# Optimization experiments

Measured on AMD Instinct MI355X. Metric: run time of the kernel, lower is better.

The kernel has to match this reference:

```python
import jax, jax.numpy as jnp
import numpy as np

N_RES, N_SSE, N_DOM = 20000, 2000, 40
E_RES, E_SSE, E_DOM = 300000, 8000, 160
F_IN, H, D, OUT = 1302, 4, 128, 256
SSE_IN = D + 3 + 1
NEG_SLOPE = 0.2   # PyG GATConv default negative_slope
BN_EPS = 1e-5


def setup_inputs() -> dict:
    key = jax.random.key(0)
    ks = jax.random.split(key, 20)
    p = lambda i, shape: jax.random.normal(ks[i], shape, dtype=jnp.float32) * 0.05
    return {
        'x_res': jax.random.normal(ks[0], (N_RES, F_IN), dtype=jnp.float32),
        'edge_index_res': jax.random.randint(ks[1], (2, E_RES), 0, N_RES),
        'edge_index_sse': jax.random.randint(ks[2], (2, E_SSE), 0, N_SSE),
        'edge_index_dom': jax.random.randint(ks[3], (2, E_DOM), 0, N_DOM),
        'res_sse_id': jnp.arange(N_RES) // (N_RES // N_SSE),  # contiguous SSE groups
        'sse_ss_type': jax.random.randint(ks[4], (N_SSE,), 0, 3),
        'n_dom': N_DOM,
        'W1': p(5, (F_IN, H * D)), 'a_src1': p(6, (H, D)), 'a_dst1': p(7, (H, D)), 'b1': jnp.zeros(H * D),
        'g1': jnp.ones(H * D), 'be1': jnp.zeros(H * D),
        'W2': p(8, (H * D, H * D)), 'a_src2': p(9, (H, D)), 'a_dst2': p(10, (H, D)), 'b2': jnp.zeros(D),
        'g2': jnp.ones(D), 'be2': jnp.zeros(D),
        'Ws': p(11, (SSE_IN, H * D)), 'a_srcs': p(12, (H, D)), 'a_dsts': p(13, (H, D)), 'bs': jnp.zeros(D),
        'gs': jnp.ones(D), 'bes': jnp.zeros(D),
        'Wd': p(14, (D, OUT)), 'bd': jnp.zeros(OUT), 'gd': jnp.ones(OUT), 'bed': jnp.zeros(OUT),
        'Wproj': p(15, (D, OUT)), 'bproj': jnp.zeros(OUT),
        'Wread': p(16, (2 * OUT, OUT)), 'bread': jnp.zeros(OUT),
    }


def _bn(x, g, b):
    # BatchNorm1d with batch statistics (training-mode math, dropout disabled)
    m = x.mean(0)
    v = ((x - m) ** 2).mean(0)
    return (x - m) * jax.lax.rsqrt(v + BN_EPS) * g + b


def _gat(x, src, dst, W, a_src, a_dst, bias, concat):
    # PyG GATConv: gather -> leaky_relu -> scatter-softmax over dst -> scatter-add
    N = x.shape[0]
    loops = jnp.arange(N)
    s = jnp.concatenate([src, loops])
    d = jnp.concatenate([dst, loops])
    h = (x @ W).reshape(N, H, D)               # [N,H,D]
    es = (h * a_src).sum(-1)                    # [N,H]
    ed = (h * a_dst).sum(-1)
    e = jax.nn.leaky_relu(es[s] + ed[d], NEG_SLOPE)          # [E+N,H]
    mx = jax.ops.segment_max(e, d, num_segments=N)
    ex = jnp.exp(e - mx[d])
    den = jax.ops.segment_sum(ex, d, num_segments=N)
    alpha = ex / (den[d] + 1e-16)
    out = jax.ops.segment_sum(alpha[:, :, None] * h[s], d, num_segments=N)  # [N,H,D]
    out = out.reshape(N, H * D) if concat else out.mean(1)
    return out + bias


def _gcn(x, src, dst, W, bias):
    # PyG GCNConv with symmetric normalization and self loops
    N = x.shape[0]
    loops = jnp.arange(N)
    s = jnp.concatenate([src, loops])
    d = jnp.concatenate([dst, loops])
    deg = jax.ops.segment_sum(jnp.ones(s.shape[0], x.dtype), d, num_segments=N)
    dis = jax.lax.rsqrt(jnp.maximum(deg, 1e-12))
    coef = dis[s] * dis[d]
    h = x @ W
    return jax.ops.segment_sum(coef[:, None] * h[s], d, num_segments=N) + bias


def reference(x_res, edge_index_res, res_sse_id, sse_ss_type, edge_index_sse,
              edge_index_dom, n_dom,
              W1, a_src1, a_dst1, b1, g1, be1,
              W2, a_src2, a_dst2, b2, g2, be2,
              Ws, a_srcs, a_dsts, bs, gs, bes,
              Wd, bd, gd, bed, Wproj, bproj, Wread, bread):
    n_res = x_res.shape[0]
    n_sse = sse_ss_type.shape[0]
    # --- Level 1: residue GATs ---
    x = _gat(x_res, edge_index_res[0], edge_index_res[1], W1, a_src1, a_dst1, b1, True)
    x = jax.nn.relu(_bn(x, g1, be1))
    x = _gat(x, edge_index_res[0], edge_index_res[1], W2, a_src2, a_dst2, b2, False)
    x = jax.nn.relu(_bn(x, g2, be2))
    # --- pool residues -> SSEs (segment mean + ss one-hot + relative length) ---
    cnt = jax.ops.segment_sum(jnp.ones(n_res, x.dtype), res_sse_id, num_segments=n_sse)
    pooled = jax.ops.segment_sum(x, res_sse_id, num_segments=n_sse) / jnp.maximum(cnt, 1.0)[:, None]
    onehot = jax.nn.one_hot(sse_ss_type, 3, dtype=x.dtype)
    length = (cnt / n_res)[:, None]
    x_sse = jnp.concatenate([pooled, onehot, length], axis=1)   # [N_sse, 132]
    # --- Level 2: SSE GAT (concat=False) ---
    x_sse = _gat(x_sse, edge_index_sse[0], edge_index_sse[1], Ws, a_srcs, a_dsts, bs, False)
    x_sse = jax.nn.relu(_bn(x_sse, gs, bes))
    # --- pool SSEs -> domains (equal contiguous partition, remainder to last) ---
    spd = n_sse // n_dom
    dom_id = jnp.minimum(jnp.arange(n_sse) // spd, n_dom - 1)
    dcnt = jax.ops.segment_sum(jnp.ones(n_sse, x_sse.dtype), dom_id, num_segments=n_dom)
    x_dom = jax.ops.segment_sum(x_sse, dom_id, num_segments=n_dom) / dcnt[:, None]
    # --- Level 3: domain GCN ---
    x_dom = _gcn(x_dom, edge_index_dom[0], edge_index_dom[1], Wd, bd)
    x_dom = jax.nn.relu(_bn(x_dom, gd, bed))
    # --- readout ---
    sse_global = x_sse.mean(0)                 # [128]
    sse_proj = sse_global @ Wproj + bproj      # [256]
    dom_mean = x_dom.mean(0)                   # [256]
    out = jnp.concatenate([sse_proj, dom_mean]) @ Wread + bread
    out = out / jnp.maximum(jnp.linalg.norm(out), 1e-12)
    return out
```

## Files before the change

### kernel.cpp

```cpp
#include <hip/hip_runtime.h>
#include <math.h>

#define NRES   20000
#define NSSE   2000
#define NDOM   40
#define FIN    1302
#define NHEAD  4
#define DDIM   128
#define HD     512
#define OUTD   256
#define SSEIN  132
#define BN_EPS 1e-5f
#define KP1    1312

typedef _Float16 f16;
typedef __attribute__((ext_vector_type(8))) _Float16 f16x8;
typedef __attribute__((ext_vector_type(4))) float f32x4;

__device__ __forceinline__ float leaky(float v) { return v > 0.f ? v : 0.2f * v; }

__global__ __launch_bounds__(256) void split_rows(const float* __restrict__ X,
                                                  f16* __restrict__ hi, f16* __restrict__ lo,
                                                  int M, int K, int Kpad) {
    long slots = (long)M * (Kpad >> 3);
    long stride = (long)gridDim.x * blockDim.x;
    for (long s = (long)blockIdx.x * blockDim.x + threadIdx.x; s < slots; s += stride) {
        int m = (int)(s / (Kpad >> 3));
        int kc = (int)(s % (Kpad >> 3)) << 3;
        f16x8 h, l;
#pragma unroll
        for (int j = 0; j < 8; ++j) {
            int k = kc + j;
            float v = (k < K) ? X[(long)m * K + k] : 0.f;
            f16 hh = (f16)v;
            h[j] = hh;
            l[j] = (f16)(v - (float)hh);
        }
        long o = ((long)m * Kpad + kc);
        *(f16x8*)&hi[o] = h;
        *(f16x8*)&lo[o] = l;
    }
}

__global__ __launch_bounds__(256) void split_w_t(const float* __restrict__ W,
                                                 f16* __restrict__ hi, f16* __restrict__ lo,
                                                 int K, int N, int Kpad) {
    long total = (long)N * Kpad;
    long stride = (long)gridDim.x * blockDim.x;
    for (long i = (long)blockIdx.x * blockDim.x + threadIdx.x; i < total; i += stride) {
        int n = (int)(i / Kpad), k = (int)(i % Kpad);
        float v = (k < K) ? W[(long)k * N + n] : 0.f;
        f16 h = (f16)v;
        hi[i] = h;
        lo[i] = (f16)(v - (float)h);
    }
}

__global__ __launch_bounds__(256) void bn_apply_split(const float* __restrict__ x,
                                                      const float* __restrict__ ab,
                                                      f16* __restrict__ hi, f16* __restrict__ lo,
                                                      long total, int C) {
    long stride = (long)gridDim.x * blockDim.x;
    for (long i = (long)blockIdx.x * blockDim.x + threadIdx.x; i < total; i += stride) {
        int c = (int)(i % C);
        float v = fmaxf(0.f, x[i] * ab[c] + ab[C + c]);
        f16 h = (f16)v;
        hi[i] = h;
        lo[i] = (f16)(v - (float)h);
    }
}

__global__ __launch_bounds__(256) void mfma_gemm(const f16* __restrict__ Ahi,
                                                 const f16* __restrict__ Alo,
                                                 const f16* __restrict__ Bthi,
                                                 const f16* __restrict__ Btlo,
                                                 float* __restrict__ C,
                                                 int M, int RB, int Kpad) {
    int bid = blockIdx.x;
    int xcd = bid & 7;
    int q = bid >> 3;
    int x = q & 3;
    int y = (q >> 2) * 8 + xcd;
    if (y >= RB) return;

    __shared__ f16 As[2][128][40];
    __shared__ f16 Bs[2][128][40];
    int t = threadIdx.x;
    int w = t >> 6, l = t & 63;
    int wr = w >> 1, wc = w & 1;
    int row0 = y * 128, col0 = x * 128;

    f32x4 acc[4][4] = {};

    for (int k0 = 0; k0 < Kpad; k0 += 32) {
#pragma unroll
        for (int r = 0; r < 2; ++r) {
            int s = t + (r << 8);
            int row = s >> 2, kc = (s & 3) << 3;
            int grow = row0 + row; if (grow >= M) grow = M - 1;
            long gia = (long)grow * Kpad + k0 + kc;
            *(f16x8*)&As[0][row][kc] = *(const f16x8*)&Ahi[gia];
            *(f16x8*)&As[1][row][kc] = *(const f16x8*)&Alo[gia];
            long gib = (long)(col0 + row) * Kpad + k0 + kc;
            *(f16x8*)&Bs[0][row][kc] = *(const f16x8*)&Bthi[gib];
            *(f16x8*)&Bs[1][row][kc] = *(const f16x8*)&Btlo[gib];
        }
        __syncthreads();

        int lr = l & 15, ks = (l >> 4) << 3;
        f16x8 ah[4], al[4], bh[4], bl[4];
#pragma unroll
        for (int fi = 0; fi < 4; ++fi) {
            int row = wr * 64 + fi * 16 + lr;
            ah[fi] = *(const f16x8*)&As[0][row][ks];
            al[fi] = *(const f16x8*)&As[1][row][ks];
        }
#pragma unroll
        for (int fj = 0; fj < 4; ++fj) {
            int col = wc * 64 + fj * 16 + lr;
            bh[fj] = *(const f16x8*)&Bs[0][col][ks];
            bl[fj] = *(const f16x8*)&Bs[1][col][ks];
        }
#pragma unroll
        for (int fi = 0; fi < 4; ++fi)
#pragma unroll
            for (int fj = 0; fj < 4; ++fj) {
                acc[fi][fj] = __builtin_amdgcn_mfma_f32_16x16x32_f16(ah[fi], bh[fj], acc[fi][fj], 0, 0, 0);
                acc[fi][fj] = __builtin_amdgcn_mfma_f32_16x16x32_f16(ah[fi], bl[fj], acc[fi][fj], 0, 0, 0);
                acc[fi][fj] = __builtin_amdgcn_mfma_f32_16x16x32_f16(al[fi], bh[fj], acc[fi][fj], 0, 0, 0);
            }
        __syncthreads();
    }
    int lr = l & 15, lq = l >> 4;
#pragma unroll
    for (int fi = 0; fi < 4; ++fi)
#pragma unroll
        for (int fj = 0; fj < 4; ++fj)
#pragma unroll
            for (int r = 0; r < 4; ++r) {
                int row = row0 + wr * 64 + fi * 16 + lq * 4 + r;
                int col = col0 + wc * 64 + fj * 16 + lr;
                if (row < M) C[(long)row * 512 + col] = acc[fi][fj][r];
            }
}

__global__ __launch_bounds__(256) void sgemm64(const float* __restrict__ A,
                                               const float* __restrict__ B,
                                               float* __restrict__ C,
                                               int M, int N, int K) {
    __shared__ float As[16][68];
    __shared__ float Bs[16][68];
    int t = threadIdx.x;
    int tx = t & 15, ty = t >> 4;
    int row0 = blockIdx.y * 64, col0 = blockIdx.x * 64;
    float acc[4][4] = {};
    for (int k0 = 0; k0 < K; k0 += 16) {
#pragma unroll
        for (int i = 0; i < 4; ++i) {
            int idx = t * 4 + i;
            int r = idx >> 4, kk = idx & 15;
            int gr = row0 + r, gk = k0 + kk;
            As[kk][r] = (gr < M && gk < K) ? A[(long)gr * K + gk] : 0.f;
        }
#pragma unroll
        for (int i = 0; i < 4; ++i) {
            int idx = t * 4 + i;
            int kk = idx >> 6, c = idx & 63;
            int gk = k0 + kk, gc = col0 + c;
            Bs[kk][c] = (gk < K && gc < N) ? B[(long)gk * N + gc] : 0.f;
        }
        __syncthreads();
#pragma unroll
        for (int kk = 0; kk < 16; ++kk) {
            float a[4], b[4];
#pragma unroll
            for (int i = 0; i < 4; ++i) a[i] = As[kk][ty * 4 + i];
#pragma unroll
            for (int j = 0; j < 4; ++j) b[j] = Bs[kk][tx * 4 + j];
#pragma unroll
            for (int i = 0; i < 4; ++i)
#pragma unroll
                for (int j = 0; j < 4; ++j) acc[i][j] += a[i] * b[j];
        }
        __syncthreads();
    }
#pragma unroll
    for (int i = 0; i < 4; ++i) {
        int r = row0 + ty * 4 + i;
        if (r >= M) continue;
#pragma unroll
        for (int j = 0; j < 4; ++j) {
            int c = col0 + tx * 4 + j;
            if (c < N) C[(long)r * N + c] = acc[i][j];
        }
    }
}

__global__ void count_deg(const int* __restrict__ dst, int E, int* __restrict__ deg) {
    int i = blockIdx.x * blockDim.x + threadIdx.x;
    if (i < E) atomicAdd(&deg[dst[i]], 1);
}

__global__ __launch_bounds__(256) void exclusive_scan(const int* __restrict__ deg,
                                                      int* __restrict__ row_ptr, int N) {
    __shared__ int part[256];
    __shared__ int base[257];
    int t = threadIdx.x;
    int chunk = (N + 255) / 256;
    int lo = t * chunk, hi = min(lo + chunk, N);
    if (lo > N) lo = N;
    if (hi > N) hi = N;
    int s = 0;
    for (int i = lo; i < hi; ++i) s += deg[i];
    part[t] = s;
    __syncthreads();
    if (t == 0) {
        int r = 0;
        for (int i = 0; i < 256; ++i) { base[i] = r; r += part[i]; }
        base[256] = r;
    }
    __syncthreads();
    int run = base[t];
    for (int i = lo; i < hi; ++i) { row_ptr[i] = run; run += deg[i]; }
    if (t == 0) row_ptr[N] = base[256];
}

__global__ void csr_fill(const int* __restrict__ src, const int* __restrict__ dst, int E,
                         const int* __restrict__ row_ptr, int* __restrict__ cursor,
                         int* __restrict__ col) {
    int i = blockIdx.x * blockDim.x + threadIdx.x;
    if (i < E) {
        int d = dst[i];
        int p = row_ptr[d] + atomicAdd(&cursor[d], 1);
        col[p] = src[i];
    }
}

__global__ __launch_bounds__(256) void att_scores(const float* __restrict__ h,
                                                  const float* __restrict__ asrc,
                                                  const float* __restrict__ adst,
                                                  float* __restrict__ es,
                                                  float* __restrict__ ed, int N) {
    int wid = threadIdx.x >> 6, lane = threadIdx.x & 63;
    int n = blockIdx.x * 4 + wid;
    if (n >= N) return;
    const float* hr = h + (long)n * HD;
    float ps[NHEAD], pd[NHEAD];
#pragma unroll
    for (int hh = 0; hh < NHEAD; ++hh) {
        float s = 0.f, d = 0.f;
#pragma unroll
        for (int j = 0; j < 2; ++j) {
            int c = hh * DDIM + lane + j * 64;
            float v = hr[c];
            s += v * asrc[c];
            d += v * adst[c];
        }
        ps[hh] = s; pd[hh] = d;
    }
#pragma unroll
    for (int off = 32; off > 0; off >>= 1) {
#pragma unroll
        for (int hh = 0; hh < NHEAD; ++hh) {
            ps[hh] += __shfl_xor(ps[hh], off);
            pd[hh] += __shfl_xor(pd[hh], off);
        }
    }
    if (lane == 0) {
#pragma unroll
        for (int hh = 0; hh < NHEAD; ++hh) {
            es[n * NHEAD + hh] = ps[hh];
            ed[n * NHEAD + hh] = pd[hh];
        }
    }
}

__global__ __launch_bounds__(256) void gat_aggregate(const float* __restrict__ h,
                                                     const float* __restrict__ es,
                                                     const float* __restrict__ ed,
                                                     const int* __restrict__ row_ptr,
                                                     const int* __restrict__ col,
                                                     const float* __restrict__ bias,
                                                     float* __restrict__ out,
                                                     int N, int concat) {
    int n = blockIdx.x;
    int t = threadIdx.x;
    int lane = t & 63, wid = t >> 6;
    int s0 = row_ptr[n], s1 = row_ptr[n + 1];

    float edv[NHEAD], vself[NHEAD];
#pragma unroll
    for (int hh = 0; hh < NHEAD; ++hh) {
        edv[hh] = ed[n * NHEAD + hh];
        vself[hh] = leaky(es[n * NHEAD + hh] + edv[hh]);
    }
    __shared__ float sred[4][NHEAD];
    __shared__ float m[NHEAD], den[NHEAD];

    float lm[NHEAD] = {-1e30f, -1e30f, -1e30f, -1e30f};
    for (int k = s0 + t; k < s1; k += 256) {
        int sn = col[k];
#pragma unroll
        for (int hh = 0; hh < NHEAD; ++hh)
            lm[hh] = fmaxf(lm[hh], leaky(es[sn * NHEAD + hh] + edv[hh]));
    }
#pragma unroll
    for (int off = 32; off > 0; off >>= 1)
#pragma unroll
        for (int hh = 0; hh < NHEAD; ++hh) lm[hh] = fmaxf(lm[hh], __shfl_xor(lm[hh], off));
    if (lane == 0)
#pragma unroll
        for (int hh = 0; hh < NHEAD; ++hh) sred[wid][hh] = lm[hh];
    __syncthreads();
    if (t < NHEAD) {
        float mm = vself[t];
#pragma unroll
        for (int w = 0; w < 4; ++w) mm = fmaxf(mm, sred[w][t]);
        m[t] = mm;
    }
    __syncthreads();
    float mh[NHEAD];
#pragma unroll
    for (int hh = 0; hh < NHEAD; ++hh) mh[hh] = m[hh];

    float ls[NHEAD] = {0.f, 0.f, 0.f, 0.f};
    for (int k = s0 + t; k < s1; k += 256) {
        int sn = col[k];
#pragma unroll
        for (int hh = 0; hh < NHEAD; ++hh)
            ls[hh] += expf(leaky(es[sn * NHEAD + hh] + edv[hh]) - mh[hh]);
    }
#pragma unroll
    for (int off = 32; off > 0; off >>= 1)
#pragma unroll
        for (int hh = 0; hh < NHEAD; ++hh) ls[hh] += __shfl_xor(ls[hh], off);
    if (lane == 0)
#pragma unroll
        for (int hh = 0; hh < NHEAD; ++hh) sred[wid][hh] = ls[hh];
    __syncthreads();
    if (t < NHEAD)
        den[t] = sred[0][t] + sred[1][t] + sred[2][t] + sred[3][t] + expf(vself[t] - m[t]);
    __syncthreads();
    float inv[NHEAD];
#pragma unroll
    for (int hh = 0; hh < NHEAD; ++hh) inv[hh] = 1.f / (den[hh] + 1e-16f);

    int d0 = t, d1 = t + 256;
    int h0 = t >> 7, h1 = h0 + 2;
    float acc0, acc1;
    {
        float a0 = expf(vself[h0] - mh[h0]) * inv[h0];
        float a1 = expf(vself[h1] - mh[h1]) * inv[h1];
        acc0 = a0 * h[(long)n * HD + d0];
        acc1 = a1 * h[(long)n * HD + d1];
    }
    __shared__ float alph[64 * NHEAD];
    for (int base = s0; base < s1; base += 64) {
        int cnt = min(64, s1 - base);
        if (t < cnt * NHEAD) {
            int e = t >> 2, hh = t & 3;
            int sn = col[base + e];
            float v = leaky(es[sn * NHEAD + hh] + edv[hh]);
            alph[(e << 2) | hh] = expf(v - mh[hh]) * inv[hh];
        }
        __syncthreads();
        for (int e = 0; e < cnt; ++e) {
            int sn = col[base + e];
            const float* hs = h + (long)sn * HD;
            acc0 += alph[(e << 2) | h0] * hs[d0];
            acc1 += alph[(e << 2) | h1] * hs[d1];
        }
        __syncthreads();
    }

    if (concat) {
        out[(long)n * HD + d0] = acc0 + bias[d0];
        out[(long)n * HD + d1] = acc1 + bias[d1];
    } else {
        __shared__ float accs[HD];
        accs[d0] = acc0;
        accs[d1] = acc1;
        __syncthreads();
        if (t < DDIM)
            out[(long)n * DDIM + t] =
                (accs[t] + accs[t + 128] + accs[t + 256] + accs[t + 384]) * 0.25f + bias[t];
    }
}

__global__ __launch_bounds__(256) void bn_stats(const float* __restrict__ x,
                                                float* __restrict__ sums, long total, int C) {
    long gid = (long)blockIdx.x * blockDim.x + threadIdx.x;
    long stride = (long)gridDim.x * blockDim.x;
    int c = (int)(gid % C);
    float s = 0.f, s2 = 0.f;
    for (long i = gid; i < total; i += stride) {
        float v = x[i];
        s += v; s2 += v * v;
    }
    atomicAdd(&sums[c], s);
    atomicAdd(&sums[C + c], s2);
}

__global__ void bn_finalize(const float* __restrict__ sums, const float* __restrict__ g,
                            const float* __restrict__ be, float* __restrict__ ab,
                            float invN, int C) {
    int c = blockIdx.x * blockDim.x + threadIdx.x;
    if (c < C) {
        float mean = sums[c] * invN;
        float var = sums[C + c] * invN - mean * mean;
        float sc = g[c] * rsqrtf(var + BN_EPS);
        ab[c] = sc;
        ab[C + c] = be[c] - mean * sc;
    }
}

__global__ __launch_bounds__(256) void bn_apply_relu(const float* __restrict__ x,
                                                     const float* __restrict__ ab,
                                                     float* __restrict__ y, long total, int C) {
    long gid = (long)blockIdx.x * blockDim.x + threadIdx.x;
    long stride = (long)gridDim.x * blockDim.x;
    for (long i = gid; i < total; i += stride) {
        int c = (int)(i % C);
        y[i] = fmaxf(0.f, x[i] * ab[c] + ab[C + c]);
    }
}

__global__ void count_res(const int* __restrict__ sid, float* __restrict__ cnt, int Nr) {
    int i = blockIdx.x * blockDim.x + threadIdx.x;
    if (i < Nr) atomicAdd(&cnt[sid[i]], 1.f);
}

__global__ __launch_bounds__(256) void pool_res(const float* __restrict__ x,
                                                const int* __restrict__ sid,
                                                float* __restrict__ pooled, int Nr) {
    long total = (long)Nr * DDIM;
    long stride = (long)gridDim.x * blockDim.x;
    for (long i = (long)blockIdx.x * blockDim.x + threadIdx.x; i < total; i += stride) {
        int n = (int)(i / DDIM), c = (int)(i % DDIM);
        atomicAdd(&pooled[(long)sid[n] * DDIM + c], x[i]);
    }
}

__global__ void build_xsse(const float* __restrict__ pooled, const float* __restrict__ cnt,
                           const int* __restrict__ sstype, float* __restrict__ xsse, int Ns) {
    int i = blockIdx.x * blockDim.x + threadIdx.x;
    if (i >= Ns * SSEIN) return;
    int s = i / SSEIN, j = i % SSEIN;
    float c = cnt[s];
    float v;
    if (j < DDIM) v = pooled[(long)s * DDIM + j] / fmaxf(c, 1.f);
    else if (j < DDIM + 3) v = (sstype[s] == (j - DDIM)) ? 1.f : 0.f;
    else v = c / (float)NRES;
    xsse[i] = v;
}

__global__ void pool_dom(const float* __restrict__ x, float* __restrict__ xdom) {
    int d = blockIdx.x, c = threadIdx.x;
    int spd = NSSE / NDOM;
    int r0 = d * spd;
    int r1 = (d == NDOM - 1) ? NSSE : r0 + spd;
    float acc = 0.f;
    for (int r = r0; r < r1; ++r) acc += x[(long)r * DDIM + c];
    xdom[d * DDIM + c] = acc / (float)(r1 - r0);
}

__global__ __launch_bounds__(256) void gcn_prep(const int* __restrict__ src,
                                                const int* __restrict__ dst, int E,
                                                float* __restrict__ dis) {
    __shared__ float degL[NDOM];
    int t = threadIdx.x;
    if (t < NDOM) degL[t] = 1.f;
    __syncthreads();
    for (int e = t; e < E; e += blockDim.x) atomicAdd(&degL[dst[e]], 1.f);
    __syncthreads();
    if (t < NDOM) dis[t] = rsqrtf(fmaxf(degL[t], 1e-12f));
}

__global__ void gcn_agg(const float* __restrict__ hdom, const int* __restrict__ src,
                        const int* __restrict__ dst, int E, const float* __restrict__ dis,
                        const float* __restrict__ bd, float* __restrict__ outd) {
    int n = blockIdx.x, c = threadIdx.x;
    float dn = dis[n];
    float acc = dn * dn * hdom[n * OUTD + c];
    for (int e = 0; e < E; ++e)
        if (dst[e] == n) acc += dis[src[e]] * dn * hdom[src[e] * OUTD + c];
    outd[n * OUTD + c] = acc + bd[c];
}

__global__ void bn_small_relu(const float* __restrict__ x, const float* __restrict__ g,
                              const float* __restrict__ be, float* __restrict__ y,
                              int N, int C) {
    int c = threadIdx.x;
    if (c >= C) return;
    float s = 0.f, s2 = 0.f;
#pragma unroll 8
    for (int r = 0; r < N; ++r) {
        float v = x[r * C + c];
        s += v; s2 += v * v;
    }
    float mean = s / N;
    float var = s2 / N - mean * mean;
    float sc = g[c] * rsqrtf(var + BN_EPS);
    float sh = be[c] - mean * sc;
#pragma unroll 8
    for (int r = 0; r < N; ++r) y[r * C + c] = fmaxf(0.f, x[r * C + c] * sc + sh);
}

__global__ __launch_bounds__(256) void col_sum_atomic(const float* __restrict__ x,
                                                      float* __restrict__ out,
                                                      long total, int C) {
    long gid = (long)blockIdx.x * blockDim.x + threadIdx.x;
    long stride = (long)gridDim.x * blockDim.x;
    int c = (int)(gid % C);
    float s = 0.f;
    for (long i = gid; i < total; i += stride) s += x[i];
    atomicAdd(&out[c], s);
}

__global__ __launch_bounds__(256) void readout(const float* __restrict__ sse_sum,
                                               float invNs,
                                               const float* __restrict__ xdom_bn,
                                               const float* __restrict__ Wproj,
                                               const float* __restrict__ bproj,
                                               const float* __restrict__ Wread,
                                               const float* __restrict__ bread,
                                               float* __restrict__ out) {
    int c = threadIdx.x;
    __shared__ float v[2 * OUTD];
    float s = 0.f;
#pragma unroll 8
    for (int k = 0; k < DDIM; ++k) s += sse_sum[k] * Wproj[k * OUTD + c];
    v[c] = s * invNs + bproj[c];
    float dm = 0.f;
#pragma unroll 8
    for (int r = 0; r < NDOM; ++r) dm += xdom_bn[r * OUTD + c];
    v[OUTD + c] = dm / (float)NDOM;
    __syncthreads();
    float o = bread[c];
#pragma unroll 8
    for (int k = 0; k < 2 * OUTD; ++k) o += v[k] * Wread[k * OUTD + c];
    __shared__ float sq[256];
    sq[c] = o * o;
    __syncthreads();
    for (int off = 128; off > 0; off >>= 1) {
        if (c < off) sq[c] += sq[c + off];
        __syncthreads();
    }
    float scale = 1.f / fmaxf(sqrtf(sq[0]), 1e-12f);
    out[c] = o * scale;
}

extern "C" void kernel_launch(void* const* d_in, const int* in_sizes, int n_in,
                              void* d_out, int out_size, void* d_ws, size_t ws_size,
                              hipStream_t stream) {
    const float* x_res = (const float*)d_in[0];
    const int* ei_res = (const int*)d_in[1];
    const int* ei_sse = (const int*)d_in[2];
    const int* ei_dom = (const int*)d_in[3];
    const int* res_sse_id = (const int*)d_in[4];
    const int* sse_ss = (const int*)d_in[5];
    const int E_res = in_sizes[1] / 2;
    const int E_sse = in_sizes[2] / 2;
    const int E_dom = in_sizes[3] / 2;
    const int Nr = in_sizes[4];
    const int Ns = in_sizes[5];
    const float* W1 = (const float*)d_in[7];
    const float* asrc1 = (const float*)d_in[8];
    const float* adst1 = (const float*)d_in[9];
    const float* b1 = (const float*)d_in[10];
    const float* g1 = (const float*)d_in[11];
    const float* be1 = (const float*)d_in[12];
    const float* W2 = (const float*)d_in[13];
    const float* asrc2 = (const float*)d_in[14];
    const float* adst2 = (const float*)d_in[15];
    const float* b2 = (const float*)d_in[16];
    const float* g2 = (const float*)d_in[17];
    const float* be2 = (const float*)d_in[18];
    const float* Ws = (const float*)d_in[19];
    const float* asrcs = (const float*)d_in[20];
    const float* adsts = (const float*)d_in[21];
    const float* bs = (const float*)d_in[22];
    const float* gs = (const float*)d_in[23];
    const float* bes = (const float*)d_in[24];
    const float* Wd = (const float*)d_in[25];
    const float* bd = (const float*)d_in[26];
    const float* gd = (const float*)d_in[27];
    const float* bed = (const float*)d_in[28];
    const float* Wproj = (const float*)d_in[29];
    const float* bproj = (const float*)d_in[30];
    const float* Wread = (const float*)d_in[31];
    const float* bread = (const float*)d_in[32];

    char* w = (char*)d_ws;
    size_t off = 0, need = 0;
    auto alloc = [&](size_t bytes) -> char* {
        char* p = w + off;
        size_t inc = (bytes + 255) & ~(size_t)255;
        need += inc;
        if (off + inc > ws_size) inc = (off < ws_size) ? (ws_size - off) : 0;
        off += inc;
        return p;
    };
    float* A     = (float*)alloc((size_t)Nr * HD * 4);
    float* Bb    = (float*)alloc((size_t)Nr * HD * 4);
    float* C2    = (float*)alloc((size_t)Nr * DDIM * 4);
    float* es    = (float*)alloc((size_t)Nr * NHEAD * 4);
    float* ed    = (float*)alloc((size_t)Nr * NHEAD * 4);
    int* rp_res  = (int*)alloc((size_t)(Nr + 1) * 4);
    int* col_res = (int*)alloc((size_t)E_res * 4);
    int* rp_sse  = (int*)alloc((size_t)(Ns + 1) * 4);
    int* col_sse = (int*)alloc((size_t)E_sse * 4);
    float* xsse  = (float*)alloc((size_t)Ns * SSEIN * 4);
    float* h_s   = (float*)alloc((size_t)Ns * HD * 4);
    float* xs_o  = (float*)alloc((size_t)Ns * DDIM * 4);
    float* xdom  = (float*)alloc((size_t)NDOM * DDIM * 4);
    float* hdom  = (float*)alloc((size_t)NDOM * OUTD * 4);
    float* gdom  = (float*)alloc((size_t)NDOM * OUTD * 4);
    float* gdom2 = (float*)alloc((size_t)NDOM * OUTD * 4);
    float* dis   = (float*)alloc((size_t)NDOM * 4);
    float* ab1   = (float*)alloc((size_t)2 * HD * 4);
    float* ab2   = (float*)alloc((size_t)2 * DDIM * 4);
    float* ab_s  = (float*)alloc((size_t)2 * DDIM * 4);
    char* zbase = w + off;
    int* deg_res  = (int*)alloc((size_t)Nr * 4);
    int* cur_res  = (int*)alloc((size_t)Nr * 4);
    int* deg_sse  = (int*)alloc((size_t)Ns * 4);
    int* cur_sse  = (int*)alloc((size_t)Ns * 4);
    float* cnt    = (float*)alloc((size_t)Ns * 4);
    float* pooled = (float*)alloc((size_t)Ns * DDIM * 4);
    float* bsum1  = (float*)alloc((size_t)2 * HD * 4);
    float* bsum2  = (float*)alloc((size_t)2 * DDIM * 4);
    float* bsum_s = (float*)alloc((size_t)2 * DDIM * 4);
    float* sse_g  = (float*)alloc((size_t)DDIM * 4);
    size_t zbytes = (size_t)((w + off) - zbase);
    f16* A1hi  = (f16*)alloc((size_t)Nr * KP1 * 2);
    f16* A1lo  = (f16*)alloc((size_t)Nr * KP1 * 2);
    f16* W1thi = (f16*)alloc((size_t)HD * KP1 * 2);
    f16* W1tlo = (f16*)alloc((size_t)HD * KP1 * 2);
    f16* W2thi = (f16*)alloc((size_t)HD * HD * 2);
    f16* W2tlo = (f16*)alloc((size_t)HD * HD * 2);
    f16* A2hi = A1hi;
    f16* A2lo = A1hi + (size_t)Nr * HD;
    bool use_mfma = (need <= ws_size);
    (void)n_in; (void)out_size;

    hipMemsetAsync(zbase, 0, zbytes, stream);

    const int* src_res = ei_res;
    const int* dst_res = ei_res + E_res;
    const int* src_sse = ei_sse;
    const int* dst_sse = ei_sse + E_sse;
    const int* src_dom = ei_dom;
    const int* dst_dom = ei_dom + E_dom;

    count_deg<<<(E_res + 255) / 256, 256, 0, stream>>>(dst_res, E_res, deg_res);
    exclusive_scan<<<1, 256, 0, stream>>>(deg_res, rp_res, Nr);
    csr_fill<<<(E_res + 255) / 256, 256, 0, stream>>>(src_res, dst_res, E_res, rp_res, cur_res, col_res);
    count_deg<<<(E_sse + 255) / 256, 256, 0, stream>>>(dst_sse, E_sse, deg_sse);
    exclusive_scan<<<1, 256, 0, stream>>>(deg_sse, rp_sse, Ns);
    csr_fill<<<(E_sse + 255) / 256, 256, 0, stream>>>(src_sse, dst_sse, E_sse, rp_sse, cur_sse, col_sse);

    int RB = (Nr + 127) / 128;
    int gemm_blocks = 32 * ((RB + 7) / 8);

    if (use_mfma) {
        split_rows<<<2048, 256, 0, stream>>>(x_res, A1hi, A1lo, Nr, FIN, KP1);
        split_w_t<<<512, 256, 0, stream>>>(W1, W1thi, W1tlo, FIN, HD, KP1);
        split_w_t<<<512, 256, 0, stream>>>(W2, W2thi, W2tlo, HD, HD, HD);
        mfma_gemm<<<gemm_blocks, 256, 0, stream>>>(A1hi, A1lo, W1thi, W1tlo, A, Nr, RB, KP1);
    } else {
        sgemm64<<<dim3(HD / 64, (Nr + 63) / 64), 256, 0, stream>>>(x_res, W1, A, Nr, HD, FIN);
    }
    att_scores<<<(Nr + 3) / 4, 256, 0, stream>>>(A, asrc1, adst1, es, ed, Nr);
    gat_aggregate<<<Nr, 256, 0, stream>>>(A, es, ed, rp_res, col_res, b1, Bb, Nr, 1);
    bn_stats<<<512, 256, 0, stream>>>(Bb, bsum1, (long)Nr * HD, HD);
    bn_finalize<<<2, 256, 0, stream>>>(bsum1, g1, be1, ab1, 1.f / Nr, HD);

    if (use_mfma) {
        bn_apply_split<<<2048, 256, 0, stream>>>(Bb, ab1, A2hi, A2lo, (long)Nr * HD, HD);
        mfma_gemm<<<gemm_blocks, 256, 0, stream>>>(A2hi, A2lo, W2thi, W2tlo, A, Nr, RB, HD);
    } else {
        bn_apply_relu<<<2048, 256, 0, stream>>>(Bb, ab1, Bb, (long)Nr * HD, HD);
        sgemm64<<<dim3(HD / 64, (Nr + 63) / 64), 256, 0, stream>>>(Bb, W2, A, Nr, HD, HD);
    }
    att_scores<<<(Nr + 3) / 4, 256, 0, stream>>>(A, asrc2, adst2, es, ed, Nr);
    gat_aggregate<<<Nr, 256, 0, stream>>>(A, es, ed, rp_res, col_res, b2, C2, Nr, 0);
    bn_stats<<<512, 256, 0, stream>>>(C2, bsum2, (long)Nr * DDIM, DDIM);
    bn_finalize<<<1, 128, 0, stream>>>(bsum2, g2, be2, ab2, 1.f / Nr, DDIM);
    bn_apply_relu<<<2048, 256, 0, stream>>>(C2, ab2, C2, (long)Nr * DDIM, DDIM);

    count_res<<<(Nr + 255) / 256, 256, 0, stream>>>(res_sse_id, cnt, Nr);
    pool_res<<<2048, 256, 0, stream>>>(C2, res_sse_id, pooled, Nr);
    build_xsse<<<(Ns * SSEIN + 255) / 256, 256, 0, stream>>>(pooled, cnt, sse_ss, xsse, Ns);

    sgemm64<<<dim3(HD / 64, (Ns + 63) / 64), 256, 0, stream>>>(xsse, Ws, h_s, Ns, HD, SSEIN);
    att_scores<<<(Ns + 3) / 4, 256, 0, stream>>>(h_s, asrcs, adsts, es, ed, Ns);
    gat_aggregate<<<Ns, 256, 0, stream>>>(h_s, es, ed, rp_sse, col_sse, bs, xs_o, Ns, 0);
    bn_stats<<<512, 256, 0, stream>>>(xs_o, bsum_s, (long)Ns * DDIM, DDIM);
    bn_finalize<<<1, 128, 0, stream>>>(bsum_s, gs, bes, ab_s, 1.f / Ns, DDIM);
    bn_apply_relu<<<512, 256, 0, stream>>>(xs_o, ab_s, xs_o, (long)Ns * DDIM, DDIM);

    pool_dom<<<NDOM, DDIM, 0, stream>>>(xs_o, xdom);
    sgemm64<<<dim3(OUTD / 64, 1), 256, 0, stream>>>(xdom, Wd, hdom, NDOM, OUTD, DDIM);
    gcn_prep<<<1, 256, 0, stream>>>(src_dom, dst_dom, E_dom, dis);
    gcn_agg<<<NDOM, OUTD, 0, stream>>>(hdom, src_dom, dst_dom, E_dom, dis, bd, gdom);
    bn_small_relu<<<1, OUTD, 0, stream>>>(gdom, gd, bed, gdom2, NDOM, OUTD);

    col_sum_atomic<<<128, 256, 0, stream>>>(xs_o, sse_g, (long)Ns * DDIM, DDIM);
    readout<<<1, OUTD, 0, stream>>>(sse_g, 1.f / (float)Ns, gdom2, Wproj, bproj, Wread, bread, (float*)d_out);
}
```

Measured before the change: 933.5 us.

## Fuse attention score dot products into MFMA GEMM epilogue and swizzle LDS

```diff
diff --git a/kernel.cpp b/kernel.cpp
--- a/kernel.cpp
+++ b/kernel.cpp
@@ -74,7 +74,11 @@
                                                  const f16* __restrict__ Alo,
                                                  const f16* __restrict__ Bthi,
                                                  const f16* __restrict__ Btlo,
+                                                 const float* __restrict__ asrc,
+                                                 const float* __restrict__ adst,
                                                  float* __restrict__ C,
+                                                 float* __restrict__ es,
+                                                 float* __restrict__ ed,
                                                  int M, int RB, int Kpad) {
     int bid = blockIdx.x;
     int xcd = bid & 7;
@@ -83,8 +87,8 @@
     int y = (q >> 2) * 8 + xcd;
     if (y >= RB) return;
 
-    __shared__ f16 As[2][128][40];
-    __shared__ f16 Bs[2][128][40];
+    __shared__ f16 As[2][128][32];
+    __shared__ f16 Bs[2][128][32];
     int t = threadIdx.x;
     int w = t >> 6, l = t & 63;
     int wr = w >> 1, wc = w & 1;
@@ -96,30 +100,33 @@
 #pragma unroll
         for (int r = 0; r < 2; ++r) {
             int s = t + (r << 8);
-            int row = s >> 2, kc = (s & 3) << 3;
+            int row = s >> 2, chunk = s & 3, kc = chunk << 3;
+            int sc = (chunk ^ ((row >> 1) & 3)) << 3;
             int grow = row0 + row; if (grow >= M) grow = M - 1;
             long gia = (long)grow * Kpad + k0 + kc;
-            *(f16x8*)&As[0][row][kc] = *(const f16x8*)&Ahi[gia];
-            *(f16x8*)&As[1][row][kc] = *(const f16x8*)&Alo[gia];
+            *(f16x8*)&As[0][row][sc] = *(const f16x8*)&Ahi[gia];
+            *(f16x8*)&As[1][row][sc] = *(const f16x8*)&Alo[gia];
             long gib = (long)(col0 + row) * Kpad + k0 + kc;
-            *(f16x8*)&Bs[0][row][kc] = *(const f16x8*)&Bthi[gib];
-            *(f16x8*)&Bs[1][row][kc] = *(const f16x8*)&Btlo[gib];
+            *(f16x8*)&Bs[0][row][sc] = *(const f16x8*)&Bthi[gib];
+            *(f16x8*)&Bs[1][row][sc] = *(const f16x8*)&Btlo[gib];
         }
         __syncthreads();
 
-        int lr = l & 15, ks = (l >> 4) << 3;
+        int lr = l & 15, g = l >> 4;
         f16x8 ah[4], al[4], bh[4], bl[4];
 #pragma unroll
         for (int fi = 0; fi < 4; ++fi) {
             int row = wr * 64 + fi * 16 + lr;
-            ah[fi] = *(const f16x8*)&As[0][row][ks];
-            al[fi] = *(const f16x8*)&As[1][row][ks];
+            int sg = (g ^ ((row >> 1) & 3)) << 3;
+            ah[fi] = *(const f16x8*)&As[0][row][sg];
+            al[fi] = *(const f16x8*)&As[1][row][sg];
         }
 #pragma unroll
         for (int fj = 0; fj < 4; ++fj) {
             int col = wc * 64 + fj * 16 + lr;
-            bh[fj] = *(const f16x8*)&Bs[0][col][ks];
-            bl[fj] = *(const f16x8*)&Bs[1][col][ks];
+            int sg = (g ^ ((col >> 1) & 3)) << 3;
+            bh[fj] = *(const f16x8*)&Bs[0][col][sg];
+            bl[fj] = *(const f16x8*)&Bs[1][col][sg];
         }
 #pragma unroll
         for (int fi = 0; fi < 4; ++fi)
@@ -131,6 +138,7 @@
             }
         __syncthreads();
     }
+
     int lr = l & 15, lq = l >> 4;
 #pragma unroll
     for (int fi = 0; fi < 4; ++fi)
@@ -142,6 +150,46 @@
                 int col = col0 + wc * 64 + fj * 16 + lr;
                 if (row < M) C[(long)row * 512 + col] = acc[fi][fj][r];
             }
+
+    float pes[4][4], ped[4][4];
+#pragma unroll
+    for (int fi = 0; fi < 4; ++fi)
+#pragma unroll
+        for (int r = 0; r < 4; ++r) { pes[fi][r] = 0.f; ped[fi][r] = 0.f; }
+#pragma unroll
+    for (int fj = 0; fj < 4; ++fj) {
+        int col = col0 + wc * 64 + fj * 16 + lr;
+        float as_ = asrc[col], ad_ = adst[col];
+#pragma unroll
+        for (int fi = 0; fi < 4; ++fi)
+#pragma unroll
+            for (int r = 0; r < 4; ++r) {
+                float v = acc[fi][fj][r];
+                pes[fi][r] += v * as_;
+                ped[fi][r] += v * ad_;
+            }
+    }
+#pragma unroll
+    for (int m = 1; m <= 8; m <<= 1)
+#pragma unroll
+        for (int fi = 0; fi < 4; ++fi)
+#pragma unroll
+            for (int r = 0; r < 4; ++r) {
+                pes[fi][r] += __shfl_xor(pes[fi][r], m);
+                ped[fi][r] += __shfl_xor(ped[fi][r], m);
+            }
+    if (lr == 0) {
+#pragma unroll
+        for (int fi = 0; fi < 4; ++fi)
+#pragma unroll
+            for (int r = 0; r < 4; ++r) {
+                int row = row0 + wr * 64 + fi * 16 + lq * 4 + r;
+                if (row < M) {
+                    atomicAdd(&es[row * NHEAD + x], pes[fi][r]);
+                    atomicAdd(&ed[row * NHEAD + x], ped[fi][r]);
+                }
+            }
+    }
 }
 
 __global__ __launch_bounds__(256) void sgemm64(const float* __restrict__ A,
@@ -604,8 +652,8 @@
     float* A     = (float*)alloc((size_t)Nr * HD * 4);
     float* Bb    = (float*)alloc((size_t)Nr * HD * 4);
     float* C2    = (float*)alloc((size_t)Nr * DDIM * 4);
-    float* es    = (float*)alloc((size_t)Nr * NHEAD * 4);
-    float* ed    = (float*)alloc((size_t)Nr * NHEAD * 4);
+    float* es_s  = (float*)alloc((size_t)Ns * NHEAD * 4);
+    float* ed_s  = (float*)alloc((size_t)Ns * NHEAD * 4);
     int* rp_res  = (int*)alloc((size_t)(Nr + 1) * 4);
     int* col_res = (int*)alloc((size_t)E_res * 4);
     int* rp_sse  = (int*)alloc((size_t)(Ns + 1) * 4);
@@ -632,6 +680,10 @@
     float* bsum2  = (float*)alloc((size_t)2 * DDIM * 4);
     float* bsum_s = (float*)alloc((size_t)2 * DDIM * 4);
     float* sse_g  = (float*)alloc((size_t)DDIM * 4);
+    float* es1    = (float*)alloc((size_t)Nr * NHEAD * 4);
+    float* ed1    = (float*)alloc((size_t)Nr * NHEAD * 4);
+    float* es2    = (float*)alloc((size_t)Nr * NHEAD * 4);
+    float* ed2    = (float*)alloc((size_t)Nr * NHEAD * 4);
     size_t zbytes = (size_t)((w + off) - zbase);
     f16* A1hi  = (f16*)alloc((size_t)Nr * KP1 * 2);
     f16* A1lo  = (f16*)alloc((size_t)Nr * KP1 * 2);
@@ -667,24 +719,26 @@
         split_rows<<<2048, 256, 0, stream>>>(x_res, A1hi, A1lo, Nr, FIN, KP1);
         split_w_t<<<512, 256, 0, stream>>>(W1, W1thi, W1tlo, FIN, HD, KP1);
         split_w_t<<<512, 256, 0, stream>>>(W2, W2thi, W2tlo, HD, HD, HD);
-        mfma_gemm<<<gemm_blocks, 256, 0, stream>>>(A1hi, A1lo, W1thi, W1tlo, A, Nr, RB, KP1);
+        mfma_gemm<<<gemm_blocks, 256, 0, stream>>>(A1hi, A1lo, W1thi, W1tlo, asrc1, adst1,
+                                                   A, es1, ed1, Nr, RB, KP1);
     } else {
         sgemm64<<<dim3(HD / 64, (Nr + 63) / 64), 256, 0, stream>>>(x_res, W1, A, Nr, HD, FIN);
-    }
-    att_scores<<<(Nr + 3) / 4, 256, 0, stream>>>(A, asrc1, adst1, es, ed, Nr);
-    gat_aggregate<<<Nr, 256, 0, stream>>>(A, es, ed, rp_res, col_res, b1, Bb, Nr, 1);
+        att_scores<<<(Nr + 3) / 4, 256, 0, stream>>>(A, asrc1, adst1, es1, ed1, Nr);
+    }
+    gat_aggregate<<<Nr, 256, 0, stream>>>(A, es1, ed1, rp_res, col_res, b1, Bb, Nr, 1);
     bn_stats<<<512, 256, 0, stream>>>(Bb, bsum1, (long)Nr * HD, HD);
     bn_finalize<<<2, 256, 0, stream>>>(bsum1, g1, be1, ab1, 1.f / Nr, HD);
 
     if (use_mfma) {
         bn_apply_split<<<2048, 256, 0, stream>>>(Bb, ab1, A2hi, A2lo, (long)Nr * HD, HD);
-        mfma_gemm<<<gemm_blocks, 256, 0, stream>>>(A2hi, A2lo, W2thi, W2tlo, A, Nr, RB, HD);
+        mfma_gemm<<<gemm_blocks, 256, 0, stream>>>(A2hi, A2lo, W2thi, W2tlo, asrc2, adst2,
+                                                   A, es2, ed2, Nr, RB, HD);
     } else {
         bn_apply_relu<<<2048, 256, 0, stream>>>(Bb, ab1, Bb, (long)Nr * HD, HD);
         sgemm64<<<dim3(HD / 64, (Nr + 63) / 64), 256, 0, stream>>>(Bb, W2, A, Nr, HD, HD);
-    }
-    att_scores<<<(Nr + 3) / 4, 256, 0, stream>>>(A, asrc2, adst2, es, ed, Nr);
-    gat_aggregate<<<Nr, 256, 0, stream>>>(A, es, ed, rp_res, col_res, b2, C2, Nr, 0);
+        att_scores<<<(Nr + 3) / 4, 256, 0, stream>>>(A, asrc2, adst2, es2, ed2, Nr);
+    }
+    gat_aggregate<<<Nr, 256, 0, stream>>>(A, es2, ed2, rp_res, col_res, b2, C2, Nr, 0);
     bn_stats<<<512, 256, 0, stream>>>(C2, bsum2, (long)Nr * DDIM, DDIM);
     bn_finalize<<<1, 128, 0, stream>>>(bsum2, g2, be2, ab2, 1.f / Nr, DDIM);
     bn_apply_relu<<<2048, 256, 0, stream>>>(C2, ab2, C2, (long)Nr * DDIM, DDIM);
@@ -694,8 +748,8 @@
     build_xsse<<<(Ns * SSEIN + 255) / 256, 256, 0, stream>>>(pooled, cnt, sse_ss, xsse, Ns);
 
     sgemm64<<<dim3(HD / 64, (Ns + 63) / 64), 256, 0, stream>>>(xsse, Ws, h_s, Ns, HD, SSEIN);
-    att_scores<<<(Ns + 3) / 4, 256, 0, stream>>>(h_s, asrcs, adsts, es, ed, Ns);
-    gat_aggregate<<<Ns, 256, 0, stream>>>(h_s, es, ed, rp_sse, col_sse, bs, xs_o, Ns, 0);
+    att_scores<<<(Ns + 3) / 4, 256, 0, stream>>>(h_s, asrcs, adsts, es_s, ed_s, Ns);
+    gat_aggregate<<<Ns, 256, 0, stream>>>(h_s, es_s, ed_s, rp_sse, col_sse, bs, xs_o, Ns, 0);
     bn_stats<<<512, 256, 0, stream>>>(xs_o, bsum_s, (long)Ns * DDIM, DDIM);
     bn_finalize<<<1, 128, 0, stream>>>(bsum_s, gs, bes, ab_s, 1.f / Ns, DDIM);
     bn_apply_relu<<<512, 256, 0, stream>>>(xs_o, ab_s, xs_o, (long)Ns * DDIM, DDIM);
```

New measurement: 977.7 us. 1.05x slower.
